# Optimization experiments

Measured on AMD Instinct MI355X. Metric: run time of the kernel, lower is better.

The kernel has to match this reference:

```python
import jax, jax.numpy as jnp
import numpy as np

D_MODEL = 1024
NUM_HEADS = 16
HEAD_DIM = D_MODEL // NUM_HEADS  # 64
# NOTE: the torch module passes scale=attention_head_size (NOT 1/sqrt(dh));
# we reproduce that exact math: scores are MULTIPLIED by head_dim.
SCALE = float(HEAD_DIM)

B, S = 2, 2048


def setup_inputs() -> dict:
    key = jax.random.key(0)
    ks = jax.random.split(key, 6)
    q = jax.random.normal(ks[0], (B, S, D_MODEL), dtype=jnp.float32)
    k = jax.random.normal(ks[1], (B, S, D_MODEL), dtype=jnp.float32)
    v = jax.random.normal(ks[2], (B, S, D_MODEL), dtype=jnp.float32)
    # Linear weights stored as [in, out]; scaled like typical init so the
    # (head_dim-scaled) logits stay numerically sane.
    w_std = 0.02
    Wq = jax.random.normal(ks[3], (D_MODEL, D_MODEL), dtype=jnp.float32) * w_std
    Wk = jax.random.normal(ks[4], (D_MODEL, D_MODEL), dtype=jnp.float32) * w_std
    Wv = jax.random.normal(ks[5], (D_MODEL, D_MODEL), dtype=jnp.float32) * w_std
    return {"q": q, "k": k, "v": v, "Wq": Wq, "Wk": Wk, "Wv": Wv}


def reference(q, k, v, Wq, Wk, Wv):
    Bq, Sq, _ = q.shape
    # QKV projections (qkv_bias=False), split into heads: [B, S, H, dh]
    qh = (q @ Wq).reshape(Bq, Sq, NUM_HEADS, HEAD_DIM)
    kh = (k @ Wk).reshape(Bq, Sq, NUM_HEADS, HEAD_DIM)
    vh = (v @ Wv).reshape(Bq, Sq, NUM_HEADS, HEAD_DIM)
    # Full materialized scores [B, H, Sq, Sk] -- the naive MHA pattern.
    sims = jnp.einsum("bqhd,bkhd->bhqk", qh, kh) * SCALE
    attn = jax.nn.softmax(sims, axis=-1)
    # Second matmul, then merge heads back: [B, S, D]
    out = jnp.einsum("bhqk,bkhd->bqhd", attn, vh).reshape(Bq, Sq, D_MODEL)
    return out
```

## Files before the change

### kernel.cpp

```cpp
#include <hip/hip_runtime.h>
#include <cstdint>
#include <cstddef>

typedef unsigned short u16;
typedef __bf16 bf16x8 __attribute__((ext_vector_type(8)));
typedef float f32x4 __attribute__((ext_vector_type(4)));
typedef unsigned int u32x4 __attribute__((ext_vector_type(4)));
typedef unsigned int u32x2 __attribute__((ext_vector_type(2)));
typedef u16 u16x4 __attribute__((ext_vector_type(4)));

typedef __attribute__((address_space(3))) void lds_void;
typedef __attribute__((address_space(1))) void glb_void;

constexpr float CEXP = 92.33248261689366f;

constexpr size_t XSZ = 4096ull * 1024ull;
constexpr size_t WSZ = 1024ull * 1024ull;
constexpr size_t OFF_XQH = 0;
constexpr size_t OFF_XQL = OFF_XQH + XSZ;
constexpr size_t OFF_XKH = OFF_XQL + XSZ;
constexpr size_t OFF_XKL = OFF_XKH + XSZ;
constexpr size_t OFF_XVH = OFF_XKL + XSZ;
constexpr size_t OFF_XVL = OFF_XVH + XSZ;
constexpr size_t OFF_WQH = OFF_XVL + XSZ;
constexpr size_t OFF_WQL = OFF_WQH + WSZ;
constexpr size_t OFF_WKH = OFF_WQL + WSZ;
constexpr size_t OFF_WKL = OFF_WKH + WSZ;
constexpr size_t OFF_WVH = OFF_WKL + WSZ;
constexpr size_t OFF_WVL = OFF_WVH + WSZ;
constexpr size_t OFF_QH  = OFF_WVL + WSZ;
constexpr size_t OFF_QL  = OFF_QH + XSZ;
constexpr size_t OFF_KH  = OFF_QL + XSZ;
constexpr size_t OFF_KL  = OFF_KH + XSZ;
constexpr size_t OFF_VH  = OFF_KL + XSZ;
constexpr size_t OFF_VT  = OFF_VH + XSZ;

__device__ __forceinline__ u16 f2b(float f) {
  unsigned u = __builtin_bit_cast(unsigned, f);
  return (u16)((u + 0x7FFFu + ((u >> 16) & 1u)) >> 16);
}
__device__ __forceinline__ float b2f(u16 h) {
  return __builtin_bit_cast(float, ((unsigned)h) << 16);
}
__device__ __forceinline__ bf16x8 ld8(const u16* p) {
  return __builtin_bit_cast(bf16x8, *(const u32x4*)p);
}
__device__ __forceinline__ unsigned pk2(float a, float b) {
#if __has_builtin(__builtin_amdgcn_cvt_pk_bf16_f32)
  auto v = __builtin_amdgcn_cvt_pk_bf16_f32(a, b);
  return __builtin_bit_cast(unsigned, v);
#else
  return (unsigned)f2b(a) | ((unsigned)f2b(b) << 16);
#endif
}
__device__ __forceinline__ float ex2(float x) {
#if __has_builtin(__builtin_amdgcn_exp2f)
  return __builtin_amdgcn_exp2f(x);
#else
  return exp2f(x);
#endif
}
__device__ __forceinline__ void glds16(const u16* g, u16* l) {
  __builtin_amdgcn_global_load_lds((const glb_void*)g, (lds_void*)l, 16, 0, 0);
}
__device__ __forceinline__ int swz32(int row, int cg) {
  return row * 32 + ((cg ^ ((row >> 1) & 3)) * 8);
}
__device__ __forceinline__ int swz64(int row, int cg) {
  return row * 64 + ((cg ^ (row & 7)) * 8);
}

__global__ __launch_bounds__(256) void convert_all(const float* __restrict__ q,
                                                   const float* __restrict__ k,
                                                   const float* __restrict__ v,
                                                   const float* __restrict__ Wq,
                                                   const float* __restrict__ Wk,
                                                   const float* __restrict__ Wv,
                                                   u16* __restrict__ ws) {
  __shared__ float tile[32][33];
  int id = blockIdx.x;
  int t = threadIdx.x;
  if (id < 12288) {
    int z = id >> 12, blk = id & 4095;
    const float* in = (z == 0) ? q : (z == 1) ? k : v;
    u16* hi = ws + ((z == 0) ? OFF_XQH : (z == 1) ? OFF_XKH : OFF_XVH);
    u16* lo = ws + ((z == 0) ? OFF_XQL : (z == 1) ? OFF_XKL : OFF_XVL);
    size_t i = ((size_t)blk * 256u + t) * 4u;
    float4 vv = *(const float4*)(in + i);
    float a[4] = {vv.x, vv.y, vv.z, vv.w};
    u16x4 hv, lv;
#pragma unroll
    for (int j = 0; j < 4; ++j) {
      u16 hb = f2b(a[j]);
      hv[j] = hb;
      lv[j] = f2b(a[j] - b2f(hb));
    }
    *(u16x4*)(hi + i) = hv;
    if (z != 2) *(u16x4*)(lo + i) = lv;
  } else {
    int r0 = id - 12288;
    int z = r0 >> 10, rem = r0 & 1023;
    const float* W = (z == 0) ? Wq : (z == 1) ? Wk : Wv;
    u16* hiT = ws + ((z == 0) ? OFF_WQH : (z == 1) ? OFF_WKH : OFF_WVH);
    u16* loT = ws + ((z == 0) ? OFF_WQL : (z == 1) ? OFF_WKL : OFF_WVL);
    int n0 = (rem & 31) * 32, k0 = (rem >> 5) * 32;
    int r = t >> 3, c0 = (t & 7) * 4;
    float4 vv = *(const float4*)(W + (size_t)(k0 + r) * 1024 + n0 + c0);
    tile[r][c0] = vv.x; tile[r][c0 + 1] = vv.y; tile[r][c0 + 2] = vv.z; tile[r][c0 + 3] = vv.w;
    __syncthreads();
    u16x4 hv, lv;
#pragma unroll
    for (int j = 0; j < 4; ++j) {
      float x = tile[c0 + j][r];
      u16 hb = f2b(x);
      hv[j] = hb;
      lv[j] = f2b(x - b2f(hb));
    }
    size_t o = (size_t)(n0 + r) * 1024 + k0 + c0;
    *(u16x4*)(hiT + o) = hv;
    if (z != 2) *(u16x4*)(loT + o) = lv;
  }
}

__global__ __launch_bounds__(256, 4) void gemm_qkv(u16* __restrict__ ws) {
  __shared__ u16 sA[2][64 * 32];
  __shared__ u16 sB[2][128 * 32];
  u16* cbuf = &sB[0][0];

  int id = blockIdx.x;
  int xcd = id & 7, seq = id >> 3;
  int pair = (seq >> 3) * 8 + xcd;
  int tile_n = seq & 7;
  int z = pair >> 6;
  int tile_m = pair & 63;

  const u16 *Ah, *Al, *Bh, *Bl; u16 *Oh, *Ol; bool split;
  if (z == 0)      { Ah = ws + OFF_XQH; Al = ws + OFF_XQL; Bh = ws + OFF_WQH; Bl = ws + OFF_WQL; Oh = ws + OFF_QH; Ol = ws + OFF_QL; split = true; }
  else if (z == 1) { Ah = ws + OFF_XKH; Al = ws + OFF_XKL; Bh = ws + OFF_WKH; Bl = ws + OFF_WKL; Oh = ws + OFF_KH; Ol = ws + OFF_KL; split = true; }
  else             { Ah = ws + OFF_XVH; Al = nullptr;      Bh = ws + OFF_WVH; Bl = nullptr;      Oh = ws + OFF_VT; Ol = nullptr;    split = false; }
  float oscale = (z == 0) ? CEXP : 1.0f;
  int m0 = tile_m * 64, n0 = tile_n * 128;
  int t = threadIdx.x, lane = t & 63, wave = t >> 6;
  int quad = lane >> 4, l15 = lane & 15;
  int wm = (wave >> 1) * 32, wn = (wave & 1) * 64;
  int rl = lane >> 2, cgl = lane & 3;
  f32x4 acc[2][4] = {};

  int rowA = wave * 16 + rl;
  size_t gA = (size_t)(m0 + rowA) * 1024 + (cgl ^ ((rowA >> 1) & 3)) * 8;
  int lbA = wave * 512;
  size_t gB[2]; int lbB[2];
#pragma unroll
  for (int i = 0; i < 2; ++i) {
    int rowB = wave * 32 + i * 16 + rl;
    gB[i] = (size_t)(n0 + rowB) * 1024 + (cgl ^ ((rowB >> 1) & 3)) * 8;
    lbB[i] = wave * 1024 + i * 512;
  }

  for (int kb = 0; kb < 32; ++kb) {
    int k0 = kb * 32;
    __syncthreads();
    glds16(Ah + gA + k0, &sA[0][lbA]);
    if (split) glds16(Al + gA + k0, &sA[1][lbA]);
#pragma unroll
    for (int i = 0; i < 2; ++i) {
      glds16(Bh + gB[i] + k0, &sB[0][lbB[i]]);
      if (split) glds16(Bl + gB[i] + k0, &sB[1][lbB[i]]);
    }
    __syncthreads();
    bf16x8 afh[2], afl[2], bfh[4], bfl[4];
#pragma unroll
    for (int mt = 0; mt < 2; ++mt) {
      int ra = wm + mt * 16 + l15;
      afh[mt] = ld8(&sA[0][swz32(ra, quad)]);
      if (split) afl[mt] = ld8(&sA[1][swz32(ra, quad)]);
    }
#pragma unroll
    for (int nt = 0; nt < 4; ++nt) {
      int rb = wn + nt * 16 + l15;
      bfh[nt] = ld8(&sB[0][swz32(rb, quad)]);
      if (split) bfl[nt] = ld8(&sB[1][swz32(rb, quad)]);
    }
#pragma unroll
    for (int mt = 0; mt < 2; ++mt)
#pragma unroll
      for (int nt = 0; nt < 4; ++nt) {
        acc[mt][nt] = __builtin_amdgcn_mfma_f32_16x16x32_bf16(afh[mt], bfh[nt], acc[mt][nt], 0, 0, 0);
        if (split) {
          acc[mt][nt] = __builtin_amdgcn_mfma_f32_16x16x32_bf16(afl[mt], bfh[nt], acc[mt][nt], 0, 0, 0);
          acc[mt][nt] = __builtin_amdgcn_mfma_f32_16x16x32_bf16(afh[mt], bfl[nt], acc[mt][nt], 0, 0, 0);
        }
      }
  }
  auto epi_round = [&](u16* dst, bool lo_round) {
#pragma unroll
    for (int mt = 0; mt < 2; ++mt)
#pragma unroll
      for (int nt = 0; nt < 4; ++nt)
#pragma unroll
        for (int r = 0; r < 4; ++r) {
          int row = wm + mt * 16 + quad * 4 + r;
          int col = wn + nt * 16 + l15;
          float v = acc[mt][nt][r] * oscale;
          u16 hb = f2b(v);
          u16 val = lo_round ? f2b(v - b2f(hb)) : hb;
          cbuf[row * 128 + (((col >> 3) ^ (row & 15)) * 8) + (col & 7)] = val;
        }
    __syncthreads();
    int row = t >> 2, seg = t & 3;
    int gm = m0 + row, bb = gm >> 11, s = gm & 2047;
    int hh = (n0 >> 6) + (seg >> 1), d0 = (seg & 1) * 32;
    u16* gp = dst + ((size_t)(bb * 16 + hh) * 2048 + s) * 64 + d0;
#pragma unroll
    for (int i = 0; i < 4; ++i) {
      int phys = (seg * 4 + i) ^ (row & 15);
      *(u32x4*)(gp + i * 8) = *(const u32x4*)(&cbuf[row * 128 + phys * 8]);
    }
  };
  __syncthreads();
  if (split) {
    epi_round(Oh, false);
    __syncthreads();
    epi_round(Ol, true);
  } else {
#pragma unroll
    for (int mt = 0; mt < 2; ++mt)
#pragma unroll
      for (int nt = 0; nt < 4; ++nt)
#pragma unroll
        for (int r = 0; r < 4; ++r) {
          int row = wm + mt * 16 + quad * 4 + r;
          int col = wn + nt * 16 + l15;
          cbuf[row * 128 + (((col >> 3) ^ (row & 15)) * 8) + (col & 7)] =
              f2b(acc[mt][nt][r]);
        }
    __syncthreads();
    int col = t >> 1, sh = t & 1;
    int hg = (n0 + col) >> 6, d = (n0 + col) & 63;
    int bb = m0 >> 11, s0 = m0 & 2047;
    u16 vals[32];
#pragma unroll
    for (int i = 0; i < 32; ++i) {
      int row = sh * 32 + i;
      vals[i] = cbuf[row * 128 + (((col >> 3) ^ (row & 15)) * 8) + (col & 7)];
    }
    u16* gp = Oh + ((size_t)((bb * 16 + hg) * 64 + d)) * 2048 + s0 + sh * 32;
#pragma unroll
    for (int i = 0; i < 4; ++i)
      *(u32x4*)(gp + i * 8) = *(const u32x4*)(&vals[i * 8]);
  }
}

__global__ __launch_bounds__(256, 4) void attn(const u16* __restrict__ ws,
                                               float* __restrict__ out) {
  __shared__ u16 lkh[64 * 64];
  __shared__ u16 lkl[64 * 64];
  __shared__ u16 lvt[64 * 64];
  __shared__ u16 lp[4][16 * 64];
  const u16* Qh = ws + OFF_QH; const u16* Ql = ws + OFF_QL;
  const u16* Kh = ws + OFF_KH; const u16* Kl = ws + OFF_KL;
  const u16* Vt = ws + OFF_VT;
  int id = blockIdx.x;
  int xcd = id & 7, slot = id >> 3;
  int hh = xcd * 4 + (slot >> 5);
  int q0 = (slot & 31) * 64;
  int b = hh >> 4, h = hh & 15;
  int t = threadIdx.x, lane = t & 63, wave = t >> 6;
  int quad = lane >> 4, l15 = lane & 15;
  size_t hb = (size_t)hh * (2048 * 64);
  bf16x8 onesf;
#pragma unroll
  for (int j = 0; j < 8; ++j) onesf[j] = __builtin_bit_cast(__bf16, (u16)0x3F80);
  int qrow = q0 + wave * 16 + l15;
  bf16x8 qfh[2], qfl[2];
#pragma unroll
  for (int ks = 0; ks < 2; ++ks) {
    size_t qo = hb + (size_t)qrow * 64 + ks * 32 + quad * 8;
    qfh[ks] = ld8(Qh + qo);
    qfl[ks] = ld8(Ql + qo);
  }
  float mi = -1e30f;
  f32x4 lsum = {};
  f32x4 o[4] = {};
  int rl = lane >> 3, cgl = lane & 7;

  size_t aK[2], aV[2]; int lb[2];
#pragma unroll
  for (int i = 0; i < 2; ++i) {
    int row = wave * 16 + i * 8 + rl;
    int cgg = cgl ^ (row & 7);
    aK[i] = hb + (size_t)row * 64 + cgg * 8;
    aV[i] = hb + (size_t)row * 2048 + cgg * 8;
    lb[i] = (wave * 16 + i * 8) * 64;
  }
  int soF[2][4];
#pragma unroll
  for (int ks = 0; ks < 2; ++ks)
#pragma unroll
    for (int nt = 0; nt < 4; ++nt)
      soF[ks][nt] = swz64(nt * 16 + l15, ks * 4 + quad);
  int soP[4];
  {
    int r7 = l15 & 7;
#pragma unroll
    for (int nt = 0; nt < 4; ++nt) {
      int c = nt * 2 + (quad >> 1);
      soP[nt] = l15 * 64 + ((c ^ r7) * 8) + (quad & 1) * 4;
    }
  }
  int soPa[2];
#pragma unroll
  for (int ks = 0; ks < 2; ++ks) soPa[ks] = swz64(l15, ks * 4 + quad);
  u16* lpw = &lp[wave][0];

#pragma unroll
  for (int i = 0; i < 2; ++i) {
    glds16(Kh + aK[i], &lkh[lb[i]]);
    glds16(Kl + aK[i], &lkl[lb[i]]);
    glds16(Vt + aV[i], &lvt[lb[i]]);
  }
  __syncthreads();

  for (int kt = 0; kt < 32; ++kt) {
    u32x4 pk_[2], pl_[2], pv_[2];
    if (kt < 31) {
#pragma unroll
      for (int i = 0; i < 2; ++i) {
        pk_[i] = *(const u32x4*)(Kh + aK[i] + (kt + 1) * 4096);
        pl_[i] = *(const u32x4*)(Kl + aK[i] + (kt + 1) * 4096);
        pv_[i] = *(const u32x4*)(Vt + aV[i] + (kt + 1) * 64);
      }
    }
    f32x4 sc[4] = {};
    __builtin_amdgcn_s_setprio(1);
#pragma unroll
    for (int nt = 0; nt < 4; ++nt) {
#pragma unroll
      for (int ks = 0; ks < 2; ++ks) {
        bf16x8 kh_ = ld8(&lkh[soF[ks][nt]]);
        bf16x8 kl_ = ld8(&lkl[soF[ks][nt]]);
        sc[nt] = __builtin_amdgcn_mfma_f32_16x16x32_bf16(kh_, qfh[ks], sc[nt], 0, 0, 0);
        sc[nt] = __builtin_amdgcn_mfma_f32_16x16x32_bf16(kl_, qfh[ks], sc[nt], 0, 0, 0);
        sc[nt] = __builtin_amdgcn_mfma_f32_16x16x32_bf16(kh_, qfl[ks], sc[nt], 0, 0, 0);
      }
    }
    __builtin_amdgcn_s_setprio(0);
    float t0 = fmaxf(fmaxf(sc[0][0], sc[0][1]), sc[0][2]);
    float t1 = fmaxf(fmaxf(sc[0][3], sc[1][0]), sc[1][1]);
    float t2 = fmaxf(fmaxf(sc[1][2], sc[1][3]), sc[2][0]);
    float t3 = fmaxf(fmaxf(sc[2][1], sc[2][2]), sc[2][3]);
    float t4 = fmaxf(fmaxf(sc[3][0], sc[3][1]), sc[3][2]);
    float mx = fmaxf(fmaxf(fmaxf(t0, t1), fmaxf(t2, t3)), fmaxf(t4, sc[3][3]));
    mx = fmaxf(mx, __shfl_xor(mx, 16));
    mx = fmaxf(mx, __shfl_xor(mx, 32));
    float mi_old = mi;
    unsigned long long live = __ballot(mx > mi_old - 28.0f);
    float mn = fmaxf(mi_old, mx);
    mi = mn;
    if (live) {
      unsigned long long grew = __ballot(mx > mi_old);
#pragma unroll
      for (int nt = 0; nt < 4; ++nt) {
        unsigned u01 = pk2(ex2(sc[nt][0] - mn), ex2(sc[nt][1] - mn));
        unsigned u23 = pk2(ex2(sc[nt][2] - mn), ex2(sc[nt][3] - mn));
        *(u32x2*)(&lpw[soP[nt]]) = u32x2{u01, u23};
      }
      if (grew) {
        float alpha_s = ex2(mi_old - mn);
        float av[4];
#pragma unroll
        for (int r = 0; r < 4; ++r) av[r] = __shfl(alpha_s, quad * 4 + r);
#pragma unroll
        for (int r = 0; r < 4; ++r) {
          lsum[r] *= av[r];
          o[0][r] *= av[r]; o[1][r] *= av[r]; o[2][r] *= av[r]; o[3][r] *= av[r];
        }
      }
      asm volatile("s_waitcnt lgkmcnt(0)" ::: "memory");
      bf16x8 pa[2];
#pragma unroll
      for (int ks = 0; ks < 2; ++ks) pa[ks] = ld8(&lpw[soPa[ks]]);
      __builtin_amdgcn_s_setprio(1);
      lsum = __builtin_amdgcn_mfma_f32_16x16x32_bf16(pa[0], onesf, lsum, 0, 0, 0);
      lsum = __builtin_amdgcn_mfma_f32_16x16x32_bf16(pa[1], onesf, lsum, 0, 0, 0);
#pragma unroll
      for (int nt = 0; nt < 4; ++nt)
#pragma unroll
        for (int ks = 0; ks < 2; ++ks) {
          bf16x8 bv = ld8(&lvt[soF[ks][nt]]);
          o[nt] = __builtin_amdgcn_mfma_f32_16x16x32_bf16(pa[ks], bv, o[nt], 0, 0, 0);
        }
      __builtin_amdgcn_s_setprio(0);
    }
    __syncthreads();
    if (kt < 31) {
#pragma unroll
      for (int i = 0; i < 2; ++i) {
        *(u32x4*)(&lkh[lb[i] + lane * 8]) = pk_[i];
        *(u32x4*)(&lkl[lb[i] + lane * 8]) = pl_[i];
        *(u32x4*)(&lvt[lb[i] + lane * 8]) = pv_[i];
      }
    }
    __syncthreads();
  }
  float inv[4];
#pragma unroll
  for (int r = 0; r < 4; ++r) inv[r] = 1.0f / lsum[r];
#pragma unroll
  for (int nt = 0; nt < 4; ++nt)
#pragma unroll
    for (int r = 0; r < 4; ++r) {
      int srow = q0 + wave * 16 + quad * 4 + r;
      int d = nt * 16 + l15;
      out[(size_t)(b * 2048 + srow) * 1024 + h * 64 + d] = o[nt][r] * inv[r];
    }
}

extern "C" void kernel_launch(void* const* d_in, const int* in_sizes, int n_in,
                              void* d_out, int out_size, void* d_ws, size_t ws_size,
                              hipStream_t stream) {
  const float* q  = (const float*)d_in[0];
  const float* k  = (const float*)d_in[1];
  const float* v  = (const float*)d_in[2];
  const float* Wq = (const float*)d_in[3];
  const float* Wk = (const float*)d_in[4];
  const float* Wv = (const float*)d_in[5];
  u16* ws = (u16*)d_ws;
  float* out = (float*)d_out;

  convert_all<<<15360, 256, 0, stream>>>(q, k, v, Wq, Wk, Wv, ws);
  gemm_qkv<<<1536, 256, 0, stream>>>(ws);
  attn<<<1024, 256, 0, stream>>>(ws, out);
}
```

Before: 275.6 us.

## Skip low-order QK correction MFMAs for dead tiles; keep P in registers via transpose

Scores are first computed with only the high-bf16 K×Q product. The two correction MFMAs (Kl·Qh, Kh·Ql) run only when some row's rough max comes within a margin of its running max, so tiles that cannot contribute skip two thirds of the QK work. The P tile no longer goes through LDS: the MFMA operand order is swapped so outputs are transposed, and P is redistributed with cross-lane shuffles. The epilogue now writes float4 vectors per row. The risk is that the approximate-score skip test is a heuristic, and the shuffles add VALU cost in place of LDS round trips.

Result: no change. 278.3 us (+1.0%).

```diff
diff --git a/kernel.cpp b/kernel.cpp
--- a/kernel.cpp
+++ b/kernel.cpp
@@ -256,7 +256,6 @@
   __shared__ u16 lkh[64 * 64];
   __shared__ u16 lkl[64 * 64];
   __shared__ u16 lvt[64 * 64];
-  __shared__ u16 lp[4][16 * 64];
   const u16* Qh = ws + OFF_QH; const u16* Ql = ws + OFF_QL;
   const u16* Kh = ws + OFF_KH; const u16* Kl = ws + OFF_KL;
   const u16* Vt = ws + OFF_VT;
@@ -299,19 +298,6 @@
 #pragma unroll
     for (int nt = 0; nt < 4; ++nt)
       soF[ks][nt] = swz64(nt * 16 + l15, ks * 4 + quad);
-  int soP[4];
-  {
-    int r7 = l15 & 7;
-#pragma unroll
-    for (int nt = 0; nt < 4; ++nt) {
-      int c = nt * 2 + (quad >> 1);
-      soP[nt] = l15 * 64 + ((c ^ r7) * 8) + (quad & 1) * 4;
-    }
-  }
-  int soPa[2];
-#pragma unroll
-  for (int ks = 0; ks < 2; ++ks) soPa[ks] = swz64(l15, ks * 4 + quad);
-  u16* lpw = &lp[wave][0];
 
 #pragma unroll
   for (int i = 0; i < 2; ++i) {
@@ -334,63 +320,88 @@
     f32x4 sc[4] = {};
     __builtin_amdgcn_s_setprio(1);
 #pragma unroll
-    for (int nt = 0; nt < 4; ++nt) {
+    for (int nt = 0; nt < 4; ++nt)
 #pragma unroll
       for (int ks = 0; ks < 2; ++ks) {
         bf16x8 kh_ = ld8(&lkh[soF[ks][nt]]);
-        bf16x8 kl_ = ld8(&lkl[soF[ks][nt]]);
         sc[nt] = __builtin_amdgcn_mfma_f32_16x16x32_bf16(kh_, qfh[ks], sc[nt], 0, 0, 0);
-        sc[nt] = __builtin_amdgcn_mfma_f32_16x16x32_bf16(kl_, qfh[ks], sc[nt], 0, 0, 0);
-        sc[nt] = __builtin_amdgcn_mfma_f32_16x16x32_bf16(kh_, qfl[ks], sc[nt], 0, 0, 0);
       }
-    }
     __builtin_amdgcn_s_setprio(0);
-    float t0 = fmaxf(fmaxf(sc[0][0], sc[0][1]), sc[0][2]);
-    float t1 = fmaxf(fmaxf(sc[0][3], sc[1][0]), sc[1][1]);
-    float t2 = fmaxf(fmaxf(sc[1][2], sc[1][3]), sc[2][0]);
-    float t3 = fmaxf(fmaxf(sc[2][1], sc[2][2]), sc[2][3]);
-    float t4 = fmaxf(fmaxf(sc[3][0], sc[3][1]), sc[3][2]);
-    float mx = fmaxf(fmaxf(fmaxf(t0, t1), fmaxf(t2, t3)), fmaxf(t4, sc[3][3]));
-    mx = fmaxf(mx, __shfl_xor(mx, 16));
-    mx = fmaxf(mx, __shfl_xor(mx, 32));
-    float mi_old = mi;
-    unsigned long long live = __ballot(mx > mi_old - 28.0f);
-    float mn = fmaxf(mi_old, mx);
-    mi = mn;
-    if (live) {
-      unsigned long long grew = __ballot(mx > mi_old);
-#pragma unroll
-      for (int nt = 0; nt < 4; ++nt) {
-        unsigned u01 = pk2(ex2(sc[nt][0] - mn), ex2(sc[nt][1] - mn));
-        unsigned u23 = pk2(ex2(sc[nt][2] - mn), ex2(sc[nt][3] - mn));
-        *(u32x2*)(&lpw[soP[nt]]) = u32x2{u01, u23};
-      }
-      if (grew) {
-        float alpha_s = ex2(mi_old - mn);
-        float av[4];
-#pragma unroll
-        for (int r = 0; r < 4; ++r) av[r] = __shfl(alpha_s, quad * 4 + r);
-#pragma unroll
-        for (int r = 0; r < 4; ++r) {
-          lsum[r] *= av[r];
-          o[0][r] *= av[r]; o[1][r] *= av[r]; o[2][r] *= av[r]; o[3][r] *= av[r];
+    {
+      float t0 = fmaxf(fmaxf(sc[0][0], sc[0][1]), sc[0][2]);
+      float t1 = fmaxf(fmaxf(sc[0][3], sc[1][0]), sc[1][1]);
+      float t2 = fmaxf(fmaxf(sc[1][2], sc[1][3]), sc[2][0]);
+      float t3 = fmaxf(fmaxf(sc[2][1], sc[2][2]), sc[2][3]);
+      float t4 = fmaxf(fmaxf(sc[3][0], sc[3][1]), sc[3][2]);
+      float mxa = fmaxf(fmaxf(fmaxf(t0, t1), fmaxf(t2, t3)), fmaxf(t4, sc[3][3]));
+      mxa = fmaxf(mxa, __shfl_xor(mxa, 16));
+      mxa = fmaxf(mxa, __shfl_xor(mxa, 32));
+      if (__ballot(mxa > mi - 32.0f)) {
+        __builtin_amdgcn_s_setprio(1);
+#pragma unroll
+        for (int nt = 0; nt < 4; ++nt)
+#pragma unroll
+          for (int ks = 0; ks < 2; ++ks) {
+            bf16x8 kh_ = ld8(&lkh[soF[ks][nt]]);
+            bf16x8 kl_ = ld8(&lkl[soF[ks][nt]]);
+            sc[nt] = __builtin_amdgcn_mfma_f32_16x16x32_bf16(kl_, qfh[ks], sc[nt], 0, 0, 0);
+            sc[nt] = __builtin_amdgcn_mfma_f32_16x16x32_bf16(kh_, qfl[ks], sc[nt], 0, 0, 0);
+          }
+        __builtin_amdgcn_s_setprio(0);
+        float e0 = fmaxf(fmaxf(sc[0][0], sc[0][1]), sc[0][2]);
+        float e1 = fmaxf(fmaxf(sc[0][3], sc[1][0]), sc[1][1]);
+        float e2 = fmaxf(fmaxf(sc[1][2], sc[1][3]), sc[2][0]);
+        float e3 = fmaxf(fmaxf(sc[2][1], sc[2][2]), sc[2][3]);
+        float e4 = fmaxf(fmaxf(sc[3][0], sc[3][1]), sc[3][2]);
+        float mx = fmaxf(fmaxf(fmaxf(e0, e1), fmaxf(e2, e3)), fmaxf(e4, sc[3][3]));
+        mx = fmaxf(mx, __shfl_xor(mx, 16));
+        mx = fmaxf(mx, __shfl_xor(mx, 32));
+        float mi_old = mi;
+        unsigned long long live = __ballot(mx > mi_old - 28.0f);
+        float mn = fmaxf(mi_old, mx);
+        if (live) {
+          unsigned long long grew = __ballot(mx > mi_old);
+          unsigned u[4][2];
+#pragma unroll
+          for (int nt = 0; nt < 4; ++nt) {
+            u[nt][0] = pk2(ex2(sc[nt][0] - mn), ex2(sc[nt][1] - mn));
+            u[nt][1] = pk2(ex2(sc[nt][2] - mn), ex2(sc[nt][3] - mn));
+          }
+          if (grew) {
+            float a = ex2(mi_old - mn);
+#pragma unroll
+            for (int r = 0; r < 4; ++r) {
+              lsum[r] *= a;
+              o[0][r] *= a; o[1][r] *= a; o[2][r] *= a; o[3][r] *= a;
+            }
+          }
+          mi = mn;
+          bf16x8 pa[2];
+#pragma unroll
+          for (int ks = 0; ks < 2; ++ks) {
+            u32x4 w4;
+#pragma unroll
+            for (int w = 0; w < 4; ++w) {
+              int srcl = ((quad & 1) * 2 + (w >> 1)) * 16 + l15;
+              unsigned s0 = (unsigned)__shfl((int)u[ks * 2 + 0][w & 1], srcl);
+              unsigned s1 = (unsigned)__shfl((int)u[ks * 2 + 1][w & 1], srcl);
+              w4[w] = (quad >> 1) ? s1 : s0;
+            }
+            pa[ks] = __builtin_bit_cast(bf16x8, w4);
+          }
+          __builtin_amdgcn_s_setprio(1);
+          lsum = __builtin_amdgcn_mfma_f32_16x16x32_bf16(onesf, pa[0], lsum, 0, 0, 0);
+          lsum = __builtin_amdgcn_mfma_f32_16x16x32_bf16(onesf, pa[1], lsum, 0, 0, 0);
+#pragma unroll
+          for (int nt = 0; nt < 4; ++nt)
+#pragma unroll
+            for (int ks = 0; ks < 2; ++ks) {
+              bf16x8 bv = ld8(&lvt[soF[ks][nt]]);
+              o[nt] = __builtin_amdgcn_mfma_f32_16x16x32_bf16(bv, pa[ks], o[nt], 0, 0, 0);
+            }
+          __builtin_amdgcn_s_setprio(0);
         }
       }
-      asm volatile("s_waitcnt lgkmcnt(0)" ::: "memory");
-      bf16x8 pa[2];
-#pragma unroll
-      for (int ks = 0; ks < 2; ++ks) pa[ks] = ld8(&lpw[soPa[ks]]);
-      __builtin_amdgcn_s_setprio(1);
-      lsum = __builtin_amdgcn_mfma_f32_16x16x32_bf16(pa[0], onesf, lsum, 0, 0, 0);
-      lsum = __builtin_amdgcn_mfma_f32_16x16x32_bf16(pa[1], onesf, lsum, 0, 0, 0);
-#pragma unroll
-      for (int nt = 0; nt < 4; ++nt)
-#pragma unroll
-        for (int ks = 0; ks < 2; ++ks) {
-          bf16x8 bv = ld8(&lvt[soF[ks][nt]]);
-          o[nt] = __builtin_amdgcn_mfma_f32_16x16x32_bf16(pa[ks], bv, o[nt], 0, 0, 0);
-        }
-      __builtin_amdgcn_s_setprio(0);
     }
     __syncthreads();
     if (kt < 31) {
@@ -403,17 +414,15 @@
     }
     __syncthreads();
   }
-  float inv[4];
-#pragma unroll
-  for (int r = 0; r < 4; ++r) inv[r] = 1.0f / lsum[r];
-#pragma unroll
-  for (int nt = 0; nt < 4; ++nt)
-#pragma unroll
-    for (int r = 0; r < 4; ++r) {
-      int srow = q0 + wave * 16 + quad * 4 + r;
-      int d = nt * 16 + l15;
-      out[(size_t)(b * 2048 + srow) * 1024 + h * 64 + d] = o[nt][r] * inv[r];
-    }
+  float inv = 1.0f / lsum[0];
+  float* op = out + (size_t)(b * 2048 + q0 + wave * 16 + l15) * 1024 + h * 64;
+#pragma unroll
+  for (int nt = 0; nt < 4; ++nt) {
+    f32x4 w;
+#pragma unroll
+    for (int r = 0; r < 4; ++r) w[r] = o[nt][r] * inv;
+    *(f32x4*)(op + nt * 16 + quad * 4) = w;
+  }
 }
 
 extern "C" void kernel_launch(void* const* d_in, const int* in_sizes, int n_in,
```
